# Kernel optimization log

Hardware: AMD Instinct MI355X
Metric: run time of the kernel (lower is better)

## Reference

```python
import jax, jax.numpy as jnp
import numpy as np
import math

ROWS, COLS, N_NODES = 256, 1024, 500000


def setup_inputs() -> dict:
    key = jax.random.key(0)
    ks = jax.random.split(key, 16)
    stdv_row = 1.0 / math.sqrt(ROWS)
    u = lambda k, shape, s: jax.random.uniform(k, shape, jnp.float32, -s, s)
    return {
        "prev_Q": jax.random.normal(ks[0], (ROWS, COLS), jnp.float32),
        "prev_Z": jax.random.normal(ks[1], (N_NODES, ROWS), jnp.float32),
        "mask": jnp.zeros((N_NODES,), jnp.float32),
        "scorer": u(ks[2], (ROWS, 1), stdv_row),
        "W_u": u(ks[3], (ROWS, ROWS), stdv_row),
        "U_u": u(ks[4], (ROWS, ROWS), stdv_row),
        "b_u": jnp.zeros((ROWS, COLS), jnp.float32),
        "W_r": u(ks[5], (ROWS, ROWS), stdv_row),
        "U_r": u(ks[6], (ROWS, ROWS), stdv_row),
        "b_r": jnp.zeros((ROWS, COLS), jnp.float32),
        "W_h": u(ks[7], (ROWS, ROWS), stdv_row),
        "U_h": u(ks[8], (ROWS, ROWS), stdv_row),
        "b_h": jnp.zeros((ROWS, COLS), jnp.float32),
    }


def reference(prev_Q, prev_Z, mask, scorer, W_u, U_u, b_u, W_r, U_r, b_r, W_h, U_h, b_h):
    k = b_u.shape[1]  # cols == TopK k
    # --- TopK node selection (k <= num_nodes, no -inf masked scores) ---
    scores = (prev_Z @ scorer).ravel() / jnp.linalg.norm(scorer) + mask  # [N]
    vals, idx = jax.lax.top_k(scores, k)                                 # [k]
    # selected nodes scaled by tanh(score), then transposed -> [rows, k]
    z_topk = (prev_Z[idx] * jnp.tanh(vals)[:, None]).T
    # --- matrix GRU gates ---
    update = jax.nn.sigmoid(W_u @ z_topk + U_u @ prev_Q + b_u)
    reset = jax.nn.sigmoid(W_r @ z_topk + U_r @ prev_Q + b_r)
    h_cap = jax.nn.relu(W_h @ z_topk + U_h @ (reset * prev_Q) + b_h)
    new_Q = (1.0 - update) * prev_Q + update * h_cap
    return new_Q
```

## Files before the change

### kernel.cpp

```cpp
#include <hip/hip_runtime.h>
#include <hip/hip_bf16.h>

#define NN 500000

typedef short bf16x8 __attribute__((ext_vector_type(8)));
typedef float f32x4 __attribute__((ext_vector_type(4)));

__device__ __forceinline__ unsigned f2key(float f){
    unsigned u = __float_as_uint(f);
    return (u & 0x80000000u) ? ~u : (u | 0x80000000u);
}
__device__ __forceinline__ unsigned long long d2key(double d){
    unsigned long long u = (unsigned long long)__double_as_longlong(d);
    return (u & 0x8000000000000000ull) ? ~u : (u | 0x8000000000000000ull);
}
__device__ __forceinline__ double key2d(unsigned long long k){
    unsigned long long u = (k & 0x8000000000000000ull) ? (k & 0x7FFFFFFFFFFFFFFFull) : ~k;
    return __longlong_as_double((long long)u);
}
__device__ __forceinline__ float sigmoidf_(float x){
    return 1.0f / (1.0f + expf(-x));
}
__device__ __forceinline__ short f2bf(float x){
    __hip_bfloat16 h = __float2bfloat16(x);
    return *reinterpret_cast<short*>(&h);
}

__global__ __launch_bounds__(256) void score_transpose_kernel(
    const float* __restrict__ prev_Q, const float4* __restrict__ Z4,
    const float* __restrict__ mask, const float* __restrict__ scorer,
    double* __restrict__ scores_d, unsigned* __restrict__ hist,
    float* __restrict__ Qt)
{
    __shared__ __attribute__((aligned(16))) char smem[18448];
    int tid = threadIdx.x;
    int b = blockIdx.x;
    if (b >= 960){
        float (*tile)[65] = (float (*)[65])smem;
        int tb = b - 960;
        int n0 = (tb & 15) * 64, m0 = (tb >> 4) * 64;
        for (int rep = 0; rep < 16; ++rep){
            int lin = tid + rep * 256;
            int r = lin >> 6, c = lin & 63;
            tile[r][c] = prev_Q[(m0 + r) * 1024 + n0 + c];
        }
        __syncthreads();
        for (int rep = 0; rep < 16; ++rep){
            int lin = tid + rep * 256;
            int r = lin >> 6, c = lin & 63;
            Qt[(n0 + r) * 256 + m0 + c] = tile[c][r];
        }
        __syncthreads();
    }
    double* nred = (double*)smem;
    double* s_invn = (double*)(smem + 2048);
    unsigned* hl = (unsigned*)(smem + 2064);
    for (int i = tid; i < 4096; i += 256) hl[i] = 0u;
    {
        double v = (double)scorer[tid];
        nred[tid] = v * v;
        __syncthreads();
        for (int s = 128; s > 0; s >>= 1){
            if (tid < s) nred[tid] += nred[tid + s];
            __syncthreads();
        }
        if (tid == 0) *s_invn = 1.0 / sqrt(nred[0]);
        __syncthreads();
    }
    double invn = *s_invn;
    int sl = tid & 15;
    int sub = (tid >> 4) & 3;
    int wid = b * 4 + (tid >> 6);
    float4 s0 = *(const float4*)&scorer[sl * 4];
    float4 s1 = *(const float4*)&scorer[(sl + 16) * 4];
    float4 s2 = *(const float4*)&scorer[(sl + 32) * 4];
    float4 s3 = *(const float4*)&scorer[(sl + 48) * 4];
    for (int r = wid * 4 + sub; r < NN; r += 16384){
        const float4* zp = Z4 + (size_t)r * 64;
        float4 z0 = zp[sl], z1 = zp[sl + 16], z2 = zp[sl + 32], z3 = zp[sl + 48];
        double d = (double)z0.x * s0.x + (double)z0.y * s0.y + (double)z0.z * s0.z + (double)z0.w * s0.w
                 + (double)z1.x * s1.x + (double)z1.y * s1.y + (double)z1.z * s1.z + (double)z1.w * s1.w
                 + (double)z2.x * s2.x + (double)z2.y * s2.y + (double)z2.z * s2.z + (double)z2.w * s2.w
                 + (double)z3.x * s3.x + (double)z3.y * s3.y + (double)z3.z * s3.z + (double)z3.w * s3.w;
        d += __shfl_xor(d, 8, 16);
        d += __shfl_xor(d, 4, 16);
        d += __shfl_xor(d, 2, 16);
        d += __shfl_xor(d, 1, 16);
        if (sl == 0){
            double sd = d * invn + (double)mask[r];
            scores_d[r] = sd;
            atomicAdd(&hl[f2key((float)sd) >> 20], 1u);
        }
    }
    __syncthreads();
    for (int i = tid; i < 4096; i += 256){
        unsigned c = hl[i];
        if (c) atomicAdd(&hist[i], c);
    }
}

__global__ __launch_bounds__(256) void collect_kernel(
    const double* __restrict__ scores_d, const unsigned* __restrict__ hist,
    unsigned* __restrict__ meta,
    unsigned long long* __restrict__ ckey, unsigned* __restrict__ cidx)
{
    __shared__ unsigned hl[4096];
    __shared__ unsigned part[256];
    __shared__ unsigned s_thr;
    int tid = threadIdx.x;
    for (int i = tid; i < 4096; i += 256) hl[i] = hist[i];
    __syncthreads();
    int hi = 4096 - 16 * tid;
    unsigned s = 0;
    for (int bb = hi - 16; bb < hi; ++bb) s += hl[bb];
    part[tid] = s;
    __syncthreads();
    for (int off = 1; off < 256; off <<= 1){
        unsigned v = (tid >= off) ? part[tid - off] : 0u;
        __syncthreads();
        part[tid] += v;
        __syncthreads();
    }
    unsigned incl = part[tid];
    unsigned excl = incl - s;
    if (excl < 1024u && incl >= 1024u){
        unsigned c = excl;
        int bb;
        for (bb = hi - 1; bb >= hi - 16; --bb){
            c += hl[bb];
            if (c >= 1024u) break;
        }
        s_thr = ((unsigned)bb) << 20;
    }
    __syncthreads();
    unsigned thr = s_thr;
    int i = blockIdx.x * 256 + tid;
    if (i < NN){
        double sd = scores_d[i];
        if (f2key((float)sd) >= thr){
            unsigned p = atomicAdd(&meta[3], 1u);
            if (p < 4096u){ ckey[p] = d2key(sd); cidx[p] = (unsigned)i; }
        }
    }
}

__global__ __launch_bounds__(1024) void sort_emit_kernel(const unsigned long long* __restrict__ ckey,
                                                         const unsigned* __restrict__ cidx,
                                                         const unsigned* __restrict__ meta,
                                                         unsigned* __restrict__ sel_idx,
                                                         float* __restrict__ sel_t)
{
    __shared__ unsigned long long sk[4096];
    __shared__ unsigned si[4096];
    int t = threadIdx.x;
    unsigned n = meta[3];
    if (n > 4096u) n = 4096u;
    int m = 1024;
    while (m < (int)n) m <<= 1;
    for (int i = t; i < m; i += 1024){
        if (i < (int)n){ sk[i] = ckey[i]; si[i] = cidx[i]; }
        else           { sk[i] = 0ull;    si[i] = 0xFFFFFFFFu; }
    }
    __syncthreads();
    int m2 = m >> 1;
    for (int k = 2; k <= m; k <<= 1){
        for (int j = k >> 1; j > 0; j >>= 1){
            for (int p = t; p < m2; p += 1024){
                int i = ((p & ~(j - 1)) << 1) | (p & (j - 1));
                int ip = i | j;
                unsigned long long ka = sk[i], kb = sk[ip];
                unsigned ia = si[i], ib = si[ip];
                bool ab = (ka > kb) || (ka == kb && ia < ib);
                bool desc = ((i & k) == 0);
                bool sw = desc ? (!ab) : ab;
                if (sw){ sk[i] = kb; sk[ip] = ka; si[i] = ib; si[ip] = ia; }
            }
            __syncthreads();
        }
    }
    sel_idx[t] = si[t];
    sel_t[t] = tanhf((float)key2d(sk[t]));
}

__global__ void gather_kernel(const float4* __restrict__ Z4,
                              const unsigned* __restrict__ sel_idx,
                              const float* __restrict__ sel_t,
                              float4* __restrict__ Xc4)
{
    int lane = threadIdx.x & 63;
    int col = (blockIdx.x << 2) + (threadIdx.x >> 6);
    unsigned idx = sel_idx[col];
    float tv = sel_t[col];
    float4 z = Z4[(size_t)idx * 64 + lane];
    float4 o; o.x = z.x * tv; o.y = z.y * tv; o.z = z.z * tv; o.w = z.w * tv;
    Xc4[col * 64 + lane] = o;
}

__global__ __launch_bounds__(256) void gemm1_mfma(
    const float* __restrict__ Wu, const float* __restrict__ Uu, const float* __restrict__ bu,
    const float* __restrict__ Wr, const float* __restrict__ Ur, const float* __restrict__ br,
    const float* __restrict__ Wh, const float* __restrict__ bh,
    const float* __restrict__ Xc, const float* __restrict__ Qt, const float* __restrict__ Q,
    float* __restrict__ Umat, float* __restrict__ RQt, float* __restrict__ P3m)
{
    __shared__ short As[4096];
    __shared__ short Xs[4096];
    int g = blockIdx.z;
    int n0 = blockIdx.x * 64, m0 = blockIdx.y * 64;
    int tid = threadIdx.x;
    int l = tid & 63, w = tid >> 6;
    int q = l >> 4, c16 = l & 15;
    f32x4 acc[4];
    #pragma unroll
    for (int i = 0; i < 4; ++i) acc[i] = (f32x4){0.f, 0.f, 0.f, 0.f};
    const float* W0 = (g == 0) ? Wu : (g == 1) ? Wr : Wh;
    const float* W1 = (g == 0) ? Uu : (g == 1) ? Ur : Wh;
    int KMAX = (g == 2) ? 256 : 512;
    for (int k0 = 0; k0 < KMAX; k0 += 64){
        const float* Asrc = (k0 < 256) ? W0 : W1;
        const float* Xsrc = (k0 < 256) ? Xc : Qt;
        int koff = k0 & 255;
        #pragma unroll
        for (int i = 0; i < 4; ++i){
            int f = tid + (i << 8);
            int row = f >> 4, c = f & 15;
            float4 av = *(const float4*)&Asrc[(m0 + row) * 256 + koff + (c << 2)];
            float4 xv = *(const float4*)&Xsrc[(n0 + row) * 256 + koff + (c << 2)];
            int kb = (c << 3) ^ ((row & 7) << 4);
            short4 ah; ah.x = f2bf(av.x); ah.y = f2bf(av.y); ah.z = f2bf(av.z); ah.w = f2bf(av.w);
            short4 xh; xh.x = f2bf(xv.x); xh.y = f2bf(xv.y); xh.z = f2bf(xv.z); xh.w = f2bf(xv.w);
            *(short4*)((char*)As + row * 128 + kb) = ah;
            *(short4*)((char*)Xs + row * 128 + kb) = xh;
        }
        __syncthreads();
        int swz = (c16 & 7) << 4;
        bf16x8 a0 = *(const bf16x8*)((const char*)As + ((w << 4) + c16) * 128 + (((q << 4)     ) ^ swz));
        bf16x8 a1 = *(const bf16x8*)((const char*)As + ((w << 4) + c16) * 128 + ((64 + (q << 4)) ^ swz));
        #pragma unroll
        for (int nr = 0; nr < 4; ++nr){
            int xrow = (nr << 4) + c16;
            bf16x8 b0 = *(const bf16x8*)((const char*)Xs + xrow * 128 + (((q << 4)     ) ^ swz));
            bf16x8 b1 = *(const bf16x8*)((const char*)Xs + xrow * 128 + ((64 + (q << 4)) ^ swz));
            acc[nr] = __builtin_amdgcn_mfma_f32_16x16x32_bf16(a0, b0, acc[nr], 0, 0, 0);
            acc[nr] = __builtin_amdgcn_mfma_f32_16x16x32_bf16(a1, b1, acc[nr], 0, 0, 0);
        }
        __syncthreads();
    }
    int mrow = m0 + (w << 4) + (q << 2);
    if (g == 0){
        #pragma unroll
        for (int nr = 0; nr < 4; ++nr){
            int ncol = n0 + (nr << 4) + c16;
            #pragma unroll
            for (int r = 0; r < 4; ++r){
                int idx = (mrow + r) * 1024 + ncol;
                Umat[idx] = sigmoidf_(acc[nr][r] + bu[idx]);
            }
        }
    } else if (g == 1){
        #pragma unroll
        for (int nr = 0; nr < 4; ++nr){
            int ncol = n0 + (nr << 4) + c16;
            float4 o;
            float* op = (float*)&o;
            #pragma unroll
            for (int r = 0; r < 4; ++r){
                int idx = (mrow + r) * 1024 + ncol;
                op[r] = sigmoidf_(acc[nr][r] + br[idx]) * Q[idx];
            }
            *(float4*)&RQt[ncol * 256 + mrow] = o;
        }
    } else {
        #pragma unroll
        for (int nr = 0; nr < 4; ++nr){
            int ncol = n0 + (nr << 4) + c16;
            #pragma unroll
            for (int r = 0; r < 4; ++r){
                int idx = (mrow + r) * 1024 + ncol;
                P3m[idx] = acc[nr][r] + bh[idx];
            }
        }
    }
}

__global__ __launch_bounds__(256) void gemm2_mfma(
    const float* __restrict__ Uh, const float* __restrict__ RQt,
    const float* __restrict__ P3m, const float* __restrict__ Umat,
    const float* __restrict__ Q, float* __restrict__ out)
{
    __shared__ short As[4096];
    __shared__ short Xs[4096];
    int n0 = blockIdx.x * 64, m0 = blockIdx.y * 64;
    int tid = threadIdx.x;
    int l = tid & 63, w = tid >> 6;
    int q = l >> 4, c16 = l & 15;
    f32x4 acc[4];
    #pragma unroll
    for (int i = 0; i < 4; ++i) acc[i] = (f32x4){0.f, 0.f, 0.f, 0.f};
    for (int k0 = 0; k0 < 256; k0 += 64){
        #pragma unroll
        for (int i = 0; i < 4; ++i){
            int f = tid + (i << 8);
            int row = f >> 4, c = f & 15;
            float4 av = *(const float4*)&Uh[(m0 + row) * 256 + k0 + (c << 2)];
            float4 xv = *(const float4*)&RQt[(n0 + row) * 256 + k0 + (c << 2)];
            int kb = (c << 3) ^ ((row & 7) << 4);
            short4 ah; ah.x = f2bf(av.x); ah.y = f2bf(av.y); ah.z = f2bf(av.z); ah.w = f2bf(av.w);
            short4 xh; xh.x = f2bf(xv.x); xh.y = f2bf(xv.y); xh.z = f2bf(xv.z); xh.w = f2bf(xv.w);
            *(short4*)((char*)As + row * 128 + kb) = ah;
            *(short4*)((char*)Xs + row * 128 + kb) = xh;
        }
        __syncthreads();
        int swz = (c16 & 7) << 4;
        bf16x8 a0 = *(const bf16x8*)((const char*)As + ((w << 4) + c16) * 128 + (((q << 4)     ) ^ swz));
        bf16x8 a1 = *(const bf16x8*)((const char*)As + ((w << 4) + c16) * 128 + ((64 + (q << 4)) ^ swz));
        #pragma unroll
        for (int nr = 0; nr < 4; ++nr){
            int xrow = (nr << 4) + c16;
            bf16x8 b0 = *(const bf16x8*)((const char*)Xs + xrow * 128 + (((q << 4)     ) ^ swz));
            bf16x8 b1 = *(const bf16x8*)((const char*)Xs + xrow * 128 + ((64 + (q << 4)) ^ swz));
            acc[nr] = __builtin_amdgcn_mfma_f32_16x16x32_bf16(a0, b0, acc[nr], 0, 0, 0);
            acc[nr] = __builtin_amdgcn_mfma_f32_16x16x32_bf16(a1, b1, acc[nr], 0, 0, 0);
        }
        __syncthreads();
    }
    int mrow = m0 + (w << 4) + (q << 2);
    #pragma unroll
    for (int nr = 0; nr < 4; ++nr){
        int ncol = n0 + (nr << 4) + c16;
        #pragma unroll
        for (int r = 0; r < 4; ++r){
            int idx = (mrow + r) * 1024 + ncol;
            float h = fmaxf(acc[nr][r] + P3m[idx], 0.0f);
            float u = Umat[idx];
            float qv = Q[idx];
            out[idx] = (1.0f - u) * qv + u * h;
        }
    }
}

extern "C" void kernel_launch(void* const* d_in, const int* in_sizes, int n_in,
                              void* d_out, int out_size, void* d_ws, size_t ws_size,
                              hipStream_t stream)
{
    const float* prev_Q = (const float*)d_in[0];
    const float* prev_Z = (const float*)d_in[1];
    const float* mask   = (const float*)d_in[2];
    const float* scorer = (const float*)d_in[3];
    const float* W_u = (const float*)d_in[4];
    const float* U_u = (const float*)d_in[5];
    const float* b_u = (const float*)d_in[6];
    const float* W_r = (const float*)d_in[7];
    const float* U_r = (const float*)d_in[8];
    const float* b_r = (const float*)d_in[9];
    const float* W_h = (const float*)d_in[10];
    const float* U_h = (const float*)d_in[11];
    const float* b_h = (const float*)d_in[12];

    char* ws = (char*)d_ws;
    double*             scores_d = (double*)            (ws + 0);
    unsigned*           hist     = (unsigned*)          (ws + 4000256);
    unsigned*           meta     = (unsigned*)          (ws + 4016640);
    unsigned long long* ckey     = (unsigned long long*)(ws + 4016704);
    unsigned*           cidx     = (unsigned*)          (ws + 4049472);
    unsigned*           sel_idx  = (unsigned*)          (ws + 4065856);
    float*              sel_t    = (float*)             (ws + 4069952);
    float*              Xc       = (float*)             (ws + 4100096);
    float*              Qt       = (float*)             (ws + 5148672);
    float*              Umat     = (float*)             (ws + 6197248);
    float*              RQt      = (float*)             (ws + 7245824);
    float*              P3m     = (float*)              (ws + 8294400);

    hipMemsetAsync(ws + 4000256, 0, 16448, stream);

    hipLaunchKernelGGL(score_transpose_kernel, dim3(1024), dim3(256), 0, stream,
                       prev_Q, (const float4*)prev_Z, mask, scorer, scores_d, hist, Qt);
    hipLaunchKernelGGL(collect_kernel, dim3(1954), dim3(256), 0, stream,
                       scores_d, hist, meta, ckey, cidx);
    hipLaunchKernelGGL(sort_emit_kernel, dim3(1), dim3(1024), 0, stream,
                       ckey, cidx, meta, sel_idx, sel_t);
    hipLaunchKernelGGL(gather_kernel, dim3(256), dim3(256), 0, stream,
                       (const float4*)prev_Z, sel_idx, sel_t, (float4*)Xc);
    hipLaunchKernelGGL(gemm1_mfma, dim3(16, 4, 3), dim3(256), 0, stream,
                       W_u, U_u, b_u, W_r, U_r, b_r, W_h, b_h,
                       Xc, Qt, prev_Q, Umat, RQt, P3m);
    hipLaunchKernelGGL(gemm2_mfma, dim3(16, 4), dim3(256), 0, stream,
                       U_h, RQt, P3m, Umat, prev_Q, (float*)d_out);
}
```

Measured before the change: 198.9 us.

## Fuse collect, sort and gather into one kernel via last-block pattern

Merges the candidate collection, bitonic sort and row gather into a single kernel launch. The last block to finish collection (detected by an atomic counter) performs the sort and then gathers the selected rows directly, dropping the intermediate sel_idx/sel_t buffers. This removes two kernel launches and their gaps. In exchange, the gather now runs in one 1024-thread block instead of a wide grid, and the collect stage uses larger blocks with a longer scan.

```diff
diff --git a/kernel.cpp b/kernel.cpp
--- a/kernel.cpp
+++ b/kernel.cpp
@@ -99,65 +99,74 @@
     }
 }
 
-__global__ __launch_bounds__(256) void collect_kernel(
+__global__ __launch_bounds__(1024) void collect_sort_gather_kernel(
     const double* __restrict__ scores_d, const unsigned* __restrict__ hist,
     unsigned* __restrict__ meta,
-    unsigned long long* __restrict__ ckey, unsigned* __restrict__ cidx)
-{
-    __shared__ unsigned hl[4096];
-    __shared__ unsigned part[256];
+    unsigned long long* __restrict__ ckey, unsigned* __restrict__ cidx,
+    const float4* __restrict__ Z4, float4* __restrict__ Xc4)
+{
+    __shared__ __attribute__((aligned(16))) char smem[49152];
     __shared__ unsigned s_thr;
+    __shared__ unsigned s_last;
     int tid = threadIdx.x;
-    for (int i = tid; i < 4096; i += 256) hl[i] = hist[i];
-    __syncthreads();
-    int hi = 4096 - 16 * tid;
-    unsigned s = 0;
-    for (int bb = hi - 16; bb < hi; ++bb) s += hl[bb];
-    part[tid] = s;
-    __syncthreads();
-    for (int off = 1; off < 256; off <<= 1){
-        unsigned v = (tid >= off) ? part[tid - off] : 0u;
-        __syncthreads();
-        part[tid] += v;
-        __syncthreads();
-    }
-    unsigned incl = part[tid];
-    unsigned excl = incl - s;
-    if (excl < 1024u && incl >= 1024u){
-        unsigned c = excl;
-        int bb;
-        for (bb = hi - 1; bb >= hi - 16; --bb){
-            c += hl[bb];
-            if (c >= 1024u) break;
-        }
-        s_thr = ((unsigned)bb) << 20;
-    }
-    __syncthreads();
+    {
+        unsigned* hl = (unsigned*)smem;
+        unsigned* part = (unsigned*)(smem + 16384);
+        for (int i = tid; i < 4096; i += 1024) hl[i] = hist[i];
+        __syncthreads();
+        int hi = 4096 - 4 * tid;
+        unsigned s = hl[hi - 4] + hl[hi - 3] + hl[hi - 2] + hl[hi - 1];
+        part[tid] = s;
+        __syncthreads();
+        for (int off = 1; off < 1024; off <<= 1){
+            unsigned v = (tid >= off) ? part[tid - off] : 0u;
+            __syncthreads();
+            part[tid] += v;
+            __syncthreads();
+        }
+        unsigned incl = part[tid];
+        unsigned excl = incl - s;
+        if (excl < 1024u && incl >= 1024u){
+            unsigned c = excl;
+            int bb;
+            for (bb = hi - 1; bb >= hi - 4; --bb){
+                c += hl[bb];
+                if (c >= 1024u) break;
+            }
+            s_thr = ((unsigned)bb) << 20;
+        }
+        __syncthreads();
+    }
     unsigned thr = s_thr;
-    int i = blockIdx.x * 256 + tid;
-    if (i < NN){
-        double sd = scores_d[i];
-        if (f2key((float)sd) >= thr){
-            unsigned p = atomicAdd(&meta[3], 1u);
-            if (p < 4096u){ ckey[p] = d2key(sd); cidx[p] = (unsigned)i; }
-        }
-    }
-}
-
-__global__ __launch_bounds__(1024) void sort_emit_kernel(const unsigned long long* __restrict__ ckey,
-                                                         const unsigned* __restrict__ cidx,
-                                                         const unsigned* __restrict__ meta,
-                                                         unsigned* __restrict__ sel_idx,
-                                                         float* __restrict__ sel_t)
-{
-    __shared__ unsigned long long sk[4096];
-    __shared__ unsigned si[4096];
-    int t = threadIdx.x;
-    unsigned n = meta[3];
+    {
+        int i = blockIdx.x * 1024 + tid;
+        if (i < NN){
+            double sd = scores_d[i];
+            if (f2key((float)sd) >= thr){
+                unsigned p = atomicAdd(&meta[3], 1u);
+                if (p < 4096u){ ckey[p] = d2key(sd); cidx[p] = (unsigned)i; }
+            }
+        }
+    }
+    __syncthreads();
+    if (tid == 0){
+        __threadfence();
+        unsigned old = atomicAdd(&meta[4], 1u);
+        s_last = (old == gridDim.x - 1u) ? 1u : 0u;
+    }
+    __syncthreads();
+    if (!s_last) return;
+    __threadfence();
+    unsigned long long* sk = (unsigned long long*)smem;
+    unsigned* si = (unsigned*)(smem + 32768);
+    unsigned n;
+    if (tid == 0) s_thr = atomicAdd(&meta[3], 0u);
+    __syncthreads();
+    n = s_thr;
     if (n > 4096u) n = 4096u;
     int m = 1024;
     while (m < (int)n) m <<= 1;
-    for (int i = t; i < m; i += 1024){
+    for (int i = tid; i < m; i += 1024){
         if (i < (int)n){ sk[i] = ckey[i]; si[i] = cidx[i]; }
         else           { sk[i] = 0ull;    si[i] = 0xFFFFFFFFu; }
     }
@@ -165,7 +174,7 @@
     int m2 = m >> 1;
     for (int k = 2; k <= m; k <<= 1){
         for (int j = k >> 1; j > 0; j >>= 1){
-            for (int p = t; p < m2; p += 1024){
+            for (int p = tid; p < m2; p += 1024){
                 int i = ((p & ~(j - 1)) << 1) | (p & (j - 1));
                 int ip = i | j;
                 unsigned long long ka = sk[i], kb = sk[ip];
@@ -178,22 +187,16 @@
             __syncthreads();
         }
     }
-    sel_idx[t] = si[t];
-    sel_t[t] = tanhf((float)key2d(sk[t]));
-}
-
-__global__ void gather_kernel(const float4* __restrict__ Z4,
-                              const unsigned* __restrict__ sel_idx,
-                              const float* __restrict__ sel_t,
-                              float4* __restrict__ Xc4)
-{
-    int lane = threadIdx.x & 63;
-    int col = (blockIdx.x << 2) + (threadIdx.x >> 6);
-    unsigned idx = sel_idx[col];
-    float tv = sel_t[col];
-    float4 z = Z4[(size_t)idx * 64 + lane];
-    float4 o; o.x = z.x * tv; o.y = z.y * tv; o.z = z.z * tv; o.w = z.w * tv;
-    Xc4[col * 64 + lane] = o;
+    {
+        int l = tid & 63, w = tid >> 6;
+        for (int row = w; row < 1024; row += 16){
+            unsigned idx = si[row];
+            float tv = tanhf((float)key2d(sk[row]));
+            float4 z = Z4[(size_t)idx * 64 + l];
+            float4 o; o.x = z.x * tv; o.y = z.y * tv; o.z = z.z * tv; o.w = z.w * tv;
+            Xc4[row * 64 + l] = o;
+        }
+    }
 }
 
 __global__ __launch_bounds__(256) void gemm1_mfma(
@@ -363,24 +366,19 @@
     unsigned*           meta     = (unsigned*)          (ws + 4016640);
     unsigned long long* ckey     = (unsigned long long*)(ws + 4016704);
     unsigned*           cidx     = (unsigned*)          (ws + 4049472);
-    unsigned*           sel_idx  = (unsigned*)          (ws + 4065856);
-    float*              sel_t    = (float*)             (ws + 4069952);
     float*              Xc       = (float*)             (ws + 4100096);
     float*              Qt       = (float*)             (ws + 5148672);
     float*              Umat     = (float*)             (ws + 6197248);
     float*              RQt      = (float*)             (ws + 7245824);
-    float*              P3m     = (float*)              (ws + 8294400);
+    float*              P3m      = (float*)             (ws + 8294400);
 
     hipMemsetAsync(ws + 4000256, 0, 16448, stream);
 
     hipLaunchKernelGGL(score_transpose_kernel, dim3(1024), dim3(256), 0, stream,
                        prev_Q, (const float4*)prev_Z, mask, scorer, scores_d, hist, Qt);
-    hipLaunchKernelGGL(collect_kernel, dim3(1954), dim3(256), 0, stream,
-                       scores_d, hist, meta, ckey, cidx);
-    hipLaunchKernelGGL(sort_emit_kernel, dim3(1), dim3(1024), 0, stream,
-                       ckey, cidx, meta, sel_idx, sel_t);
-    hipLaunchKernelGGL(gather_kernel, dim3(256), dim3(256), 0, stream,
-                       (const float4*)prev_Z, sel_idx, sel_t, (float4*)Xc);
+    hipLaunchKernelGGL(collect_sort_gather_kernel, dim3(489), dim3(1024), 0, stream,
+                       scores_d, hist, meta, ckey, cidx,
+                       (const float4*)prev_Z, (float4*)Xc);
     hipLaunchKernelGGL(gemm1_mfma, dim3(16, 4, 3), dim3(256), 0, stream,
                        W_u, U_u, b_u, W_r, U_r, b_r, W_h, b_h,
                        Xc, Qt, prev_Q, Umat, RQt, P3m);
```

New measurement: 242.6 us. 1.22x slower.

## Split score pass from histogram and Q transpose into separate kernels

Applied to the files above, without the earlier changes.

Splits the fused score/transpose/histogram kernel into a pure streaming score kernel and a second kernel that builds the histogram from stored scores and transposes prev_Q. The score kernel drops its 16KB shared histogram, so more blocks can be resident. It also uses a larger grid (1536 blocks) and reorders the double-precision dot product into four partial sums to shorten the dependency chain. In exchange there is an extra launch and a re-read of the 4MB score array.

```diff
diff --git a/kernel.cpp b/kernel.cpp
--- a/kernel.cpp
+++ b/kernel.cpp
@@ -26,18 +26,71 @@
     return *reinterpret_cast<short*>(&h);
 }
 
-__global__ __launch_bounds__(256) void score_transpose_kernel(
-    const float* __restrict__ prev_Q, const float4* __restrict__ Z4,
-    const float* __restrict__ mask, const float* __restrict__ scorer,
-    double* __restrict__ scores_d, unsigned* __restrict__ hist,
-    float* __restrict__ Qt)
-{
-    __shared__ __attribute__((aligned(16))) char smem[18448];
+__global__ __launch_bounds__(256) void score_kernel(
+    const float4* __restrict__ Z4, const float* __restrict__ mask,
+    const float* __restrict__ scorer, double* __restrict__ scores_d)
+{
+    __shared__ double nred[256];
+    __shared__ double s_invn;
+    int tid = threadIdx.x;
+    {
+        double v = (double)scorer[tid];
+        nred[tid] = v * v;
+        __syncthreads();
+        for (int s = 128; s > 0; s >>= 1){
+            if (tid < s) nred[tid] += nred[tid + s];
+            __syncthreads();
+        }
+        if (tid == 0) s_invn = 1.0 / sqrt(nred[0]);
+        __syncthreads();
+    }
+    double invn = s_invn;
+    int sl = tid & 15;
+    int grp = tid >> 4;
+    int gid = blockIdx.x * 16 + grp;
+    const float4* s4 = (const float4*)scorer;
+    float4 s0 = s4[sl], s1 = s4[sl + 16], s2 = s4[sl + 32], s3 = s4[sl + 48];
+    for (int r = gid; r < NN; r += 24576){
+        const float4* zp = Z4 + (size_t)r * 64;
+        float4 z0 = zp[sl], z1 = zp[sl + 16], z2 = zp[sl + 32], z3 = zp[sl + 48];
+        double p0 = (double)z0.x * s0.x + (double)z0.y * s0.y + (double)z0.z * s0.z + (double)z0.w * s0.w;
+        double p1 = (double)z1.x * s1.x + (double)z1.y * s1.y + (double)z1.z * s1.z + (double)z1.w * s1.w;
+        double p2 = (double)z2.x * s2.x + (double)z2.y * s2.y + (double)z2.z * s2.z + (double)z2.w * s2.w;
+        double p3 = (double)z3.x * s3.x + (double)z3.y * s3.y + (double)z3.z * s3.z + (double)z3.w * s3.w;
+        double d = (p0 + p1) + (p2 + p3);
+        d += __shfl_xor(d, 8, 16);
+        d += __shfl_xor(d, 4, 16);
+        d += __shfl_xor(d, 2, 16);
+        d += __shfl_xor(d, 1, 16);
+        if (sl == 0){
+            scores_d[r] = d * invn + (double)mask[r];
+        }
+    }
+}
+
+__global__ __launch_bounds__(256) void hist_transpose_kernel(
+    const double* __restrict__ scores_d, unsigned* __restrict__ hist,
+    const float* __restrict__ prev_Q, float* __restrict__ Qt)
+{
+    __shared__ __attribute__((aligned(16))) char smem[16640];
     int tid = threadIdx.x;
     int b = blockIdx.x;
-    if (b >= 960){
+    if (b < 256){
+        unsigned* h = (unsigned*)smem;
+        for (int i = tid; i < 4096; i += 256) h[i] = 0u;
+        __syncthreads();
+        for (int i = b * 256 + tid; i < NN; i += 65536){
+            double sd = scores_d[i];
+            atomicAdd(&h[f2key((float)sd) >> 20], 1u);
+        }
+        __syncthreads();
+        for (int i = tid; i < 4096; i += 256){
+            unsigned c = h[i];
+            if (c) atomicAdd(&hist[i], c);
+        }
+    } else {
         float (*tile)[65] = (float (*)[65])smem;
-        int tb = b - 960;
+        int tb = b - 256;
         int n0 = (tb & 15) * 64, m0 = (tb >> 4) * 64;
         for (int rep = 0; rep < 16; ++rep){
             int lin = tid + rep * 256;
@@ -50,52 +103,6 @@
             int r = lin >> 6, c = lin & 63;
             Qt[(n0 + r) * 256 + m0 + c] = tile[c][r];
         }
-        __syncthreads();
-    }
-    double* nred = (double*)smem;
-    double* s_invn = (double*)(smem + 2048);
-    unsigned* hl = (unsigned*)(smem + 2064);
-    for (int i = tid; i < 4096; i += 256) hl[i] = 0u;
-    {
-        double v = (double)scorer[tid];
-        nred[tid] = v * v;
-        __syncthreads();
-        for (int s = 128; s > 0; s >>= 1){
-            if (tid < s) nred[tid] += nred[tid + s];
-            __syncthreads();
-        }
-        if (tid == 0) *s_invn = 1.0 / sqrt(nred[0]);
-        __syncthreads();
-    }
-    double invn = *s_invn;
-    int sl = tid & 15;
-    int sub = (tid >> 4) & 3;
-    int wid = b * 4 + (tid >> 6);
-    float4 s0 = *(const float4*)&scorer[sl * 4];
-    float4 s1 = *(const float4*)&scorer[(sl + 16) * 4];
-    float4 s2 = *(const float4*)&scorer[(sl + 32) * 4];
-    float4 s3 = *(const float4*)&scorer[(sl + 48) * 4];
-    for (int r = wid * 4 + sub; r < NN; r += 16384){
-        const float4* zp = Z4 + (size_t)r * 64;
-        float4 z0 = zp[sl], z1 = zp[sl + 16], z2 = zp[sl + 32], z3 = zp[sl + 48];
-        double d = (double)z0.x * s0.x + (double)z0.y * s0.y + (double)z0.z * s0.z + (double)z0.w * s0.w
-                 + (double)z1.x * s1.x + (double)z1.y * s1.y + (double)z1.z * s1.z + (double)z1.w * s1.w
-                 + (double)z2.x * s2.x + (double)z2.y * s2.y + (double)z2.z * s2.z + (double)z2.w * s2.w
-                 + (double)z3.x * s3.x + (double)z3.y * s3.y + (double)z3.z * s3.z + (double)z3.w * s3.w;
-        d += __shfl_xor(d, 8, 16);
-        d += __shfl_xor(d, 4, 16);
-        d += __shfl_xor(d, 2, 16);
-        d += __shfl_xor(d, 1, 16);
-        if (sl == 0){
-            double sd = d * invn + (double)mask[r];
-            scores_d[r] = sd;
-            atomicAdd(&hl[f2key((float)sd) >> 20], 1u);
-        }
-    }
-    __syncthreads();
-    for (int i = tid; i < 4096; i += 256){
-        unsigned c = hl[i];
-        if (c) atomicAdd(&hist[i], c);
     }
 }
 
@@ -369,12 +376,14 @@
     float*              Qt       = (float*)             (ws + 5148672);
     float*              Umat     = (float*)             (ws + 6197248);
     float*              RQt      = (float*)             (ws + 7245824);
-    float*              P3m     = (float*)              (ws + 8294400);
+    float*              P3m      = (float*)             (ws + 8294400);
 
     hipMemsetAsync(ws + 4000256, 0, 16448, stream);
 
-    hipLaunchKernelGGL(score_transpose_kernel, dim3(1024), dim3(256), 0, stream,
-                       prev_Q, (const float4*)prev_Z, mask, scorer, scores_d, hist, Qt);
+    hipLaunchKernelGGL(score_kernel, dim3(1536), dim3(256), 0, stream,
+                       (const float4*)prev_Z, mask, scorer, scores_d);
+    hipLaunchKernelGGL(hist_transpose_kernel, dim3(320), dim3(256), 0, stream,
+                       scores_d, hist, prev_Q, Qt);
     hipLaunchKernelGGL(collect_kernel, dim3(1954), dim3(256), 0, stream,
                        scores_d, hist, meta, ckey, cidx);
     hipLaunchKernelGGL(sort_emit_kernel, dim3(1), dim3(1024), 0, stream,
```

New measurement: 199.0 us. About the same (+0.0%).
